# Kernel tuning notes

Measured on AMD Instinct MI355X. Metric: run time of the kernel, lower is better.

## Reference

```python
import jax, jax.numpy as jnp
import numpy as np
import math

DIM = 1024
K = 3
NUM_LAYERS = 1
RES_SCALE = 1.0 / math.sqrt(NUM_LAYERS)


def rmsnorm(x, gamma):
    # F.normalize(x, dim=-1) * sqrt(dim) * (gamma + 1)
    n = jnp.sqrt(jnp.sum(x * x, axis=-1, keepdims=True))
    return x / jnp.maximum(n, 1e-12) * (x.shape[-1] ** 0.5) * (gamma + 1.0)


def causal_dwconv(x, w_dw, b_dw, w_pw, b_pw):
    # x: [B, L, D]; w_dw: [D, 1, K]; w_pw: [D, D]
    xt = jnp.transpose(x, (0, 2, 1))                     # [B, D, L]
    xt = jnp.pad(xt, ((0, 0), (0, 0), (K - 1, 0)))       # causal left pad
    y = jax.lax.conv_general_dilated(
        xt, w_dw, window_strides=(1,), padding='VALID',
        feature_group_count=xt.shape[1],
        dimension_numbers=('NCH', 'OIH', 'NCH'))          # [B, D, L]
    y = y + b_dw[None, :, None]
    y = jnp.transpose(y, (0, 2, 1))                       # [B, L, D]
    return jnp.einsum('bld,ed->ble', y, w_pw) + b_pw      # 1x1 conv


def log_g(x):
    return jnp.where(x >= 0, jnp.log(jax.nn.relu(x) + 0.5), -jax.nn.softplus(-x))


def heinsen_scan_log(log_coeffs, log_values):
    # h_t = exp(a*_t + logcumsumexp(log_values - a*))
    a_star = jnp.cumsum(log_coeffs, axis=1)
    log_h = a_star + jax.lax.cumlogsumexp(log_values - a_star, axis=1)
    return jnp.exp(log_h)


def min_gru(x, w_hg):
    # x: [B, L, D]; w_hg: [2D, D] (no bias, expansion_factor=1 -> to_out is identity)
    hg = jnp.einsum('bld,ed->ble', x, w_hg)
    hidden, gate = jnp.split(hg, 2, axis=-1)
    log_coeffs = -jax.nn.softplus(gate)        # log(1 - z)
    log_values = -jax.nn.softplus(-gate) + log_g(hidden)  # log z + log g(h~)
    out = heinsen_scan_log(log_coeffs, log_values)         # [B, L, D]
    next_hidden = out[:, -1:]
    return out, next_hidden


def setup_inputs() -> dict:
    key = jax.random.key(0)
    ks = jax.random.split(key, 12)
    D = DIM
    s = 0.02
    return {
        'x': jax.random.normal(ks[0], (4, 4096, D), jnp.float32),
        'conv_dw_w': jax.random.normal(ks[1], (D, 1, K), jnp.float32) * s,
        'conv_dw_b': jax.random.normal(ks[2], (D,), jnp.float32) * s,
        'conv_pw_w': jax.random.normal(ks[3], (D, D), jnp.float32) * s,
        'conv_pw_b': jax.random.normal(ks[4], (D,), jnp.float32) * s,
        'conv_norm_g': jax.random.normal(ks[5], (D,), jnp.float32) * s,
        'gru_norm_g': jax.random.normal(ks[6], (D,), jnp.float32) * s,
        'gru_w': jax.random.normal(ks[7], (2 * D, D), jnp.float32) * s,
        'ff_norm_g': jax.random.normal(ks[8], (D,), jnp.float32) * s,
        'ff_w1': jax.random.normal(ks[9], (4 * D, D), jnp.float32) * s,
        'ff_b1': jax.random.normal(ks[10], (4 * D,), jnp.float32) * s,
        'ff_w2': jax.random.normal(ks[11], (D, 4 * D), jnp.float32) * s,
        'ff_b2': jnp.zeros((D,), jnp.float32),
    }


def reference(x, conv_dw_w, conv_dw_b, conv_pw_w, conv_pw_b, conv_norm_g,
              gru_norm_g, gru_w, ff_norm_g, ff_w1, ff_b1, ff_w2, ff_b2):
    # Conv branch (residual)
    x = causal_dwconv(rmsnorm(x, conv_norm_g), conv_dw_w, conv_dw_b,
                      conv_pw_w, conv_pw_b) * RES_SCALE + x
    # MinGRU branch (residual); dropout is identity at inference
    gru_out, next_hidden = min_gru(rmsnorm(x, gru_norm_g), gru_w)
    x = gru_out * RES_SCALE + x
    # FeedForward branch (residual), exact GELU
    h = rmsnorm(x, ff_norm_g)
    h = jax.nn.gelu(jnp.einsum('bld,ed->ble', h, ff_w1) + ff_b1, approximate=False)
    h = jnp.einsum('ble,de->bld', h, ff_w2) + ff_b2
    x = h * RES_SCALE + x
    return x, next_hidden
```

## Files before the change

kernel.cpp:

```cpp
#include <hip/hip_runtime.h>

typedef __attribute__((ext_vector_type(8))) short short8;
typedef __attribute__((ext_vector_type(4))) float floatx4;

#define D_   1024
#define L_   4096
#define B_   4
#define T_   16384
#define NCH  32
#define CHL  128

__device__ __forceinline__ ushort f2bf(float f) {
  unsigned u = __float_as_uint(f);
  u += 0x7fffu + ((u >> 16) & 1u);
  return (ushort)(u >> 16);
}
__device__ __forceinline__ float bf2f(ushort u) {
  return __uint_as_float(((unsigned)u) << 16);
}

__device__ __forceinline__ void gl2lds(const ushort* g, ushort* l) {
  __builtin_amdgcn_global_load_lds(
      (const __attribute__((address_space(1))) unsigned int*)g,
      (__attribute__((address_space(3))) unsigned int*)l, 16, 0, 0);
}

__global__ __launch_bounds__(256) void cvt_bf(const float* __restrict__ s,
                                              ushort* __restrict__ d, int n4) {
  int i = blockIdx.x * 256 + threadIdx.x;
  if (i >= n4) return;
  float4 v = ((const float4*)s)[i];
  ushort4 o;
  o.x = f2bf(v.x); o.y = f2bf(v.y); o.z = f2bf(v.z); o.w = f2bf(v.w);
  ((ushort4*)d)[i] = o;
}

__global__ __launch_bounds__(256) void rms_reduce(const float* __restrict__ x,
                                                  float* __restrict__ inv) {
  int t = blockIdx.x;
  float4 v = ((const float4*)(x + (size_t)t * D_))[threadIdx.x];
  float s = v.x * v.x + v.y * v.y + v.z * v.z + v.w * v.w;
#pragma unroll
  for (int off = 32; off > 0; off >>= 1) s += __shfl_xor(s, off, 64);
  __shared__ float red[4];
  if ((threadIdx.x & 63) == 0) red[threadIdx.x >> 6] = s;
  __syncthreads();
  if (threadIdx.x == 0)
    inv[t] = 32.0f / fmaxf(sqrtf(red[0] + red[1] + red[2] + red[3]), 1e-12f);
}

__global__ __launch_bounds__(256) void rms_scale(const float* __restrict__ x,
                                                 const float* __restrict__ g,
                                                 ushort* __restrict__ z) {
  int t = blockIdx.x;
  float4 v = ((const float4*)(x + (size_t)t * D_))[threadIdx.x];
  float s = v.x * v.x + v.y * v.y + v.z * v.z + v.w * v.w;
#pragma unroll
  for (int off = 32; off > 0; off >>= 1) s += __shfl_xor(s, off, 64);
  __shared__ float red[4];
  if ((threadIdx.x & 63) == 0) red[threadIdx.x >> 6] = s;
  __syncthreads();
  float iv = 32.0f / fmaxf(sqrtf(red[0] + red[1] + red[2] + red[3]), 1e-12f);
  float4 gg = ((const float4*)g)[threadIdx.x];
  ushort4 o;
  o.x = f2bf(v.x * iv * (gg.x + 1.f));
  o.y = f2bf(v.y * iv * (gg.y + 1.f));
  o.z = f2bf(v.z * iv * (gg.z + 1.f));
  o.w = f2bf(v.w * iv * (gg.w + 1.f));
  ((ushort4*)(z + (size_t)t * D_))[threadIdx.x] = o;
}

__global__ __launch_bounds__(256) void dwconv_k(const float* __restrict__ x,
                                                const float* __restrict__ inv,
                                                const float* __restrict__ wdw,
                                                const float* __restrict__ bdw,
                                                const float* __restrict__ gm,
                                                ushort* __restrict__ y) {
  int t = blockIdx.x;
  int c4 = threadIdx.x << 2;
  int l = t & (L_ - 1);
  const float* p0 = x + (size_t)t * D_ + c4;
  float i0 = inv[t], i1 = 0.f, i2 = 0.f;
  float4 v0 = *(const float4*)p0;
  float4 v1 = {0.f, 0.f, 0.f, 0.f}, v2 = {0.f, 0.f, 0.f, 0.f};
  if (l >= 1) { v1 = *(const float4*)(p0 - D_);     i1 = inv[t - 1]; }
  if (l >= 2) { v2 = *(const float4*)(p0 - 2 * D_); i2 = inv[t - 2]; }
  float a0[4] = {v0.x, v0.y, v0.z, v0.w};
  float a1[4] = {v1.x, v1.y, v1.z, v1.w};
  float a2[4] = {v2.x, v2.y, v2.z, v2.w};
  ushort r[4];
#pragma unroll
  for (int j = 0; j < 4; ++j) {
    int d = c4 + j;
    float w0 = wdw[d * 3 + 0], w1 = wdw[d * 3 + 1], w2 = wdw[d * 3 + 2];
    float s = w2 * a0[j] * i0 + w1 * a1[j] * i1 + w0 * a2[j] * i2;
    s = s * (gm[d] + 1.0f) + bdw[d];
    r[j] = f2bf(s);
  }
  ushort4 o; o.x = r[0]; o.y = r[1]; o.z = r[2]; o.w = r[3];
  *(ushort4*)(y + (size_t)t * D_ + c4) = o;
}

template <int MODE>
__global__ __launch_bounds__(256, 2) void gemm_k(
    const ushort* __restrict__ A, const ushort* __restrict__ W,
    const float* __restrict__ bias, const float* __restrict__ resid,
    float* __restrict__ outF, ushort* __restrict__ outB, int M, int N, int K) {
  __shared__ ushort lA[128 * 32];
  __shared__ ushort lB[128 * 32];
  int tid = threadIdx.x;

  int nx = gridDim.x;
  int lxs = 31 - __clz(nx);
  int lin = blockIdx.x + blockIdx.y * nx;
  int c = lin & 7, q = lin >> 3;
  int by = (c * (gridDim.y >> 3)) + (q >> lxs);
  int bx = q & (nx - 1);
  int bm = by * 128;
  int bn = bx * 128;

  int wave = tid >> 6, lane = tid & 63;
  int wm = (wave & 1) << 6, wn = (wave >> 1) << 6;
  int row = tid >> 2, kc = (tid & 3) << 3;
  const ushort* pa0 = A + (size_t)(bm + row) * K + kc;
  const ushort* pa1 = pa0 + (size_t)64 * K;
  const ushort* pb0 = W + (size_t)(bn + row) * K + kc;
  const ushort* pb1 = pb0 + (size_t)64 * K;
  ushort* dA0 = lA + tid * 8;
  ushort* dA1 = dA0 + 64 * 32;
  ushort* dB0 = lB + tid * 8;
  ushort* dB1 = dB0 + 64 * 32;
  int fr = lane & 15, fq = lane >> 4;

  floatx4 acc[4][4];
#pragma unroll
  for (int i = 0; i < 4; ++i)
#pragma unroll
    for (int j = 0; j < 4; ++j) acc[i][j] = {0.f, 0.f, 0.f, 0.f};

  for (int k0 = 0; k0 < K; k0 += 32) {
    __syncthreads();
    gl2lds(pa0 + k0, dA0);
    gl2lds(pa1 + k0, dA1);
    gl2lds(pb0 + k0, dB0);
    gl2lds(pb1 + k0, dB1);
    __syncthreads();
    short8 af[4], bfr[4];
#pragma unroll
    for (int i = 0; i < 4; ++i)
      af[i] = *(const short8*)(lA + (wm + i * 16 + fr) * 32 + fq * 8);
#pragma unroll
    for (int j = 0; j < 4; ++j)
      bfr[j] = *(const short8*)(lB + (wn + j * 16 + fr) * 32 + fq * 8);
#pragma unroll
    for (int i = 0; i < 4; ++i)
#pragma unroll
      for (int j = 0; j < 4; ++j)
        acc[i][j] = __builtin_amdgcn_mfma_f32_16x16x32_bf16(af[i], bfr[j], acc[i][j], 0, 0, 0);
  }

#pragma unroll
  for (int i = 0; i < 4; ++i) {
#pragma unroll
    for (int j = 0; j < 4; ++j) {
      int colg = bn + wn + j * 16 + fr;
      float bv = (MODE == 3) ? 0.f : bias[colg];
#pragma unroll
      for (int r = 0; r < 4; ++r) {
        int rowg = bm + wm + i * 16 + fq * 4 + r;
        size_t idx = (size_t)rowg * N + colg;
        float v = acc[i][j][r];
        if (MODE == 0) {
          outF[idx] = v + bv + resid[idx];
        } else if (MODE == 2) {
          v += bv;
          v = 0.5f * v * (1.0f + erff(v * 0.70710678118f));
          outB[idx] = f2bf(v);
        } else {
          outB[idx] = f2bf(v);
        }
      }
    }
  }
}

__device__ __forceinline__ void gates(float hid, float gt, float& a, float& bv) {
  a = 1.f / (1.f + __expf(gt));
  float sg = 1.f / (1.f + __expf(-gt));
  float g = (hid >= 0.f) ? (hid + 0.5f) : (1.f / (1.f + __expf(-hid)));
  bv = sg * g;
}

__global__ __launch_bounds__(256) void scan_p1(const ushort* __restrict__ hg,
                                               float* __restrict__ Ag,
                                               float* __restrict__ Bg) {
  int blk = blockIdx.x;
  int dt = blk & 3, ch = (blk >> 2) & 31, b = blk >> 7;
  int d = (dt << 8) + threadIdx.x;
  const ushort* p = hg + (size_t)(b * L_ + ch * CHL) * 2048 + d;
  float A = 1.f, Bv = 0.f;
  for (int s = 0; s < CHL; ++s) {
    float hid = bf2f(p[0]), gt = bf2f(p[1024]);
    p += 2048;
    float a, bv; gates(hid, gt, a, bv);
    A *= a;
    Bv = fmaf(a, Bv, bv);
  }
  size_t o = (size_t)((b * NCH + ch) * D_) + d;
  Ag[o] = A; Bg[o] = Bv;
}

__global__ __launch_bounds__(256) void scan_p2(const float* __restrict__ Ag,
                                               const float* __restrict__ Bg,
                                               float* __restrict__ Pre) {
  int dt = blockIdx.x & 3, b = blockIdx.x >> 2;
  int d = (dt << 8) + threadIdx.x;
  float h = 0.f;
  for (int c = 0; c < NCH; ++c) {
    size_t i = (size_t)((b * NCH + c) * D_) + d;
    Pre[i] = h;
    h = fmaf(Ag[i], h, Bg[i]);
  }
}

__global__ __launch_bounds__(256) void scan_p3(const ushort* __restrict__ hg,
                                               const float* __restrict__ Pre,
                                               float* __restrict__ xio,
                                               float* __restrict__ nh) {
  int blk = blockIdx.x;
  int dt = blk & 3, ch = (blk >> 2) & 31, b = blk >> 7;
  int d = (dt << 8) + threadIdx.x;
  const ushort* p = hg + (size_t)(b * L_ + ch * CHL) * 2048 + d;
  float* q = xio + (size_t)(b * L_ + ch * CHL) * D_ + d;
  float h = Pre[(size_t)((b * NCH + ch) * D_) + d];
  for (int s = 0; s < CHL; ++s) {
    float hid = bf2f(p[0]), gt = bf2f(p[1024]);
    p += 2048;
    float a, bv; gates(hid, gt, a, bv);
    h = fmaf(a, h, bv);
    *q = h + *q;
    q += D_;
  }
  if (ch == NCH - 1) nh[(b << 10) + d] = h;
}

extern "C" void kernel_launch(void* const* d_in, const int* in_sizes, int n_in,
                              void* d_out, int out_size, void* d_ws, size_t ws_size,
                              hipStream_t stream) {
  const float* x   = (const float*)d_in[0];
  const float* cdw = (const float*)d_in[1];
  const float* cdb = (const float*)d_in[2];
  const float* cpw = (const float*)d_in[3];
  const float* cpb = (const float*)d_in[4];
  const float* cng = (const float*)d_in[5];
  const float* gng = (const float*)d_in[6];
  const float* gw  = (const float*)d_in[7];
  const float* fng = (const float*)d_in[8];
  const float* fw1 = (const float*)d_in[9];
  const float* fb1 = (const float*)d_in[10];
  const float* fw2 = (const float*)d_in[11];
  const float* fb2 = (const float*)d_in[12];
  float* out = (float*)d_out;
  char* ws = (char*)d_ws;

  ushort* wpw_b = (ushort*)(ws + 0);
  ushort* wgr_b = (ushort*)(ws + 2097152);
  ushort* wf1_b = (ushort*)(ws + 6291456);
  ushort* wf2_b = (ushort*)(ws + 14680064);
  float*  inv   = (float*) (ws + 23068672);
  float*  Ag    = (float*) (ws + 23134208);
  float*  Bg    = (float*) (ws + 23658496);
  float*  Pre   = (float*) (ws + 24182784);
  ushort* zbuf  = (ushort*)(ws + 24707072);
  ushort* hg    = (ushort*)(ws + 58261504);
  ushort* h1    = (ushort*)(ws + 58261504);
  float*  nh    = out + (size_t)T_ * D_;

  cvt_bf<<<dim3(1024), 256, 0, stream>>>(cpw, wpw_b, 262144);
  cvt_bf<<<dim3(2048), 256, 0, stream>>>(gw,  wgr_b, 524288);
  cvt_bf<<<dim3(4096), 256, 0, stream>>>(fw1, wf1_b, 1048576);
  cvt_bf<<<dim3(4096), 256, 0, stream>>>(fw2, wf2_b, 1048576);

  rms_reduce<<<dim3(T_), 256, 0, stream>>>(x, inv);
  dwconv_k<<<dim3(T_), 256, 0, stream>>>(x, inv, cdw, cdb, cng, zbuf);
  gemm_k<0><<<dim3(8, 128), 256, 0, stream>>>(zbuf, wpw_b, cpb, x, out, nullptr, T_, 1024, 1024);

  rms_scale<<<dim3(T_), 256, 0, stream>>>(out, gng, zbuf);
  gemm_k<3><<<dim3(16, 128), 256, 0, stream>>>(zbuf, wgr_b, nullptr, nullptr, nullptr, hg, T_, 2048, 1024);
  scan_p1<<<dim3(512), 256, 0, stream>>>(hg, Ag, Bg);
  scan_p2<<<dim3(16), 256, 0, stream>>>(Ag, Bg, Pre);
  scan_p3<<<dim3(512), 256, 0, stream>>>(hg, Pre, out, nh);

  rms_scale<<<dim3(T_), 256, 0, stream>>>(out, fng, zbuf);
  gemm_k<2><<<dim3(32, 128), 256, 0, stream>>>(zbuf, wf1_b, fb1, nullptr, nullptr, h1, T_, 4096, 1024);
  gemm_k<0><<<dim3(8, 128), 256, 0, stream>>>(h1, wf2_b, fb2, out, out, nullptr, T_, 1024, 4096);
}
```

Baseline: 838.0 us.

## Fuse RMS reduction into dwconv, move minGRU gates into GEMM epilogue, approximate GELU

Drops the separate rms_reduce pass: dwconv now recomputes the norms of the current and two previous rows through block reductions. The minGRU gate nonlinearities move into the gate GEMM epilogue, which stores g(h) and the coefficient a in bf16, so both scan passes read them directly instead of evaluating exponentials twice. Exact erf-based GELU is replaced by the tanh-form approximation written as a sigmoid. This cuts memory passes and transcendental work, but adds a numerical deviation from the exact GELU and stores the gate coefficient at bf16 precision.

```diff
diff --git a/kernel.cpp b/kernel.cpp
--- a/kernel.cpp
+++ b/kernel.cpp
@@ -33,20 +33,6 @@
   ushort4 o;
   o.x = f2bf(v.x); o.y = f2bf(v.y); o.z = f2bf(v.z); o.w = f2bf(v.w);
   ((ushort4*)d)[i] = o;
-}
-
-__global__ __launch_bounds__(256) void rms_reduce(const float* __restrict__ x,
-                                                  float* __restrict__ inv) {
-  int t = blockIdx.x;
-  float4 v = ((const float4*)(x + (size_t)t * D_))[threadIdx.x];
-  float s = v.x * v.x + v.y * v.y + v.z * v.z + v.w * v.w;
-#pragma unroll
-  for (int off = 32; off > 0; off >>= 1) s += __shfl_xor(s, off, 64);
-  __shared__ float red[4];
-  if ((threadIdx.x & 63) == 0) red[threadIdx.x >> 6] = s;
-  __syncthreads();
-  if (threadIdx.x == 0)
-    inv[t] = 32.0f / fmaxf(sqrtf(red[0] + red[1] + red[2] + red[3]), 1e-12f);
 }
 
 __global__ __launch_bounds__(256) void rms_scale(const float* __restrict__ x,
@@ -71,7 +57,6 @@
 }
 
 __global__ __launch_bounds__(256) void dwconv_k(const float* __restrict__ x,
-                                                const float* __restrict__ inv,
                                                 const float* __restrict__ wdw,
                                                 const float* __restrict__ bdw,
                                                 const float* __restrict__ gm,
@@ -80,11 +65,28 @@
   int c4 = threadIdx.x << 2;
   int l = t & (L_ - 1);
   const float* p0 = x + (size_t)t * D_ + c4;
-  float i0 = inv[t], i1 = 0.f, i2 = 0.f;
   float4 v0 = *(const float4*)p0;
   float4 v1 = {0.f, 0.f, 0.f, 0.f}, v2 = {0.f, 0.f, 0.f, 0.f};
-  if (l >= 1) { v1 = *(const float4*)(p0 - D_);     i1 = inv[t - 1]; }
-  if (l >= 2) { v2 = *(const float4*)(p0 - 2 * D_); i2 = inv[t - 2]; }
+  if (l >= 1) v1 = *(const float4*)(p0 - D_);
+  if (l >= 2) v2 = *(const float4*)(p0 - 2 * D_);
+  float s0 = v0.x * v0.x + v0.y * v0.y + v0.z * v0.z + v0.w * v0.w;
+  float s1 = v1.x * v1.x + v1.y * v1.y + v1.z * v1.z + v1.w * v1.w;
+  float s2 = v2.x * v2.x + v2.y * v2.y + v2.z * v2.z + v2.w * v2.w;
+#pragma unroll
+  for (int off = 32; off > 0; off >>= 1) {
+    s0 += __shfl_xor(s0, off, 64);
+    s1 += __shfl_xor(s1, off, 64);
+    s2 += __shfl_xor(s2, off, 64);
+  }
+  __shared__ float r0[4], r1[4], r2[4];
+  if ((threadIdx.x & 63) == 0) {
+    int w = threadIdx.x >> 6;
+    r0[w] = s0; r1[w] = s1; r2[w] = s2;
+  }
+  __syncthreads();
+  float i0 = 32.0f / fmaxf(sqrtf(r0[0] + r0[1] + r0[2] + r0[3]), 1e-12f);
+  float i1 = 32.0f / fmaxf(sqrtf(r1[0] + r1[1] + r1[2] + r1[3]), 1e-12f);
+  float i2 = 32.0f / fmaxf(sqrtf(r2[0] + r2[1] + r2[2] + r2[3]), 1e-12f);
   float a0[4] = {v0.x, v0.y, v0.z, v0.w};
   float a1[4] = {v1.x, v1.y, v1.z, v1.w};
   float a2[4] = {v2.x, v2.y, v2.z, v2.w};
@@ -164,7 +166,7 @@
 #pragma unroll
     for (int j = 0; j < 4; ++j) {
       int colg = bn + wn + j * 16 + fr;
-      float bv = (MODE == 3) ? 0.f : bias[colg];
+      float bv = (MODE == 4) ? 0.f : bias[colg];
 #pragma unroll
       for (int r = 0; r < 4; ++r) {
         int rowg = bm + wm + i * 16 + fq * 4 + r;
@@ -174,21 +176,20 @@
           outF[idx] = v + bv + resid[idx];
         } else if (MODE == 2) {
           v += bv;
-          v = 0.5f * v * (1.0f + erff(v * 0.70710678118f));
+          float u = 1.5957691216f * (v + 0.044715f * v * v * v);
+          v = v / (1.f + __expf(-u));
           outB[idx] = f2bf(v);
         } else {
-          outB[idx] = f2bf(v);
+          float o;
+          if (colg < 1024)
+            o = (v >= 0.f) ? (v + 0.5f) : (1.f / (1.f + __expf(-v)));
+          else
+            o = 1.f / (1.f + __expf(v));
+          outB[idx] = f2bf(o);
         }
       }
     }
   }
-}
-
-__device__ __forceinline__ void gates(float hid, float gt, float& a, float& bv) {
-  a = 1.f / (1.f + __expf(gt));
-  float sg = 1.f / (1.f + __expf(-gt));
-  float g = (hid >= 0.f) ? (hid + 0.5f) : (1.f / (1.f + __expf(-hid)));
-  bv = sg * g;
 }
 
 __global__ __launch_bounds__(256) void scan_p1(const ushort* __restrict__ hg,
@@ -200,11 +201,10 @@
   const ushort* p = hg + (size_t)(b * L_ + ch * CHL) * 2048 + d;
   float A = 1.f, Bv = 0.f;
   for (int s = 0; s < CHL; ++s) {
-    float hid = bf2f(p[0]), gt = bf2f(p[1024]);
+    float g = bf2f(p[0]), a = bf2f(p[1024]);
     p += 2048;
-    float a, bv; gates(hid, gt, a, bv);
     A *= a;
-    Bv = fmaf(a, Bv, bv);
+    Bv = fmaf(a, Bv, (1.f - a) * g);
   }
   size_t o = (size_t)((b * NCH + ch) * D_) + d;
   Ag[o] = A; Bg[o] = Bv;
@@ -234,10 +234,9 @@
   float* q = xio + (size_t)(b * L_ + ch * CHL) * D_ + d;
   float h = Pre[(size_t)((b * NCH + ch) * D_) + d];
   for (int s = 0; s < CHL; ++s) {
-    float hid = bf2f(p[0]), gt = bf2f(p[1024]);
+    float g = bf2f(p[0]), a = bf2f(p[1024]);
     p += 2048;
-    float a, bv; gates(hid, gt, a, bv);
-    h = fmaf(a, h, bv);
+    h = fmaf(a, h, (1.f - a) * g);
     *q = h + *q;
     q += D_;
   }
@@ -267,7 +266,6 @@
   ushort* wgr_b = (ushort*)(ws + 2097152);
   ushort* wf1_b = (ushort*)(ws + 6291456);
   ushort* wf2_b = (ushort*)(ws + 14680064);
-  float*  inv   = (float*) (ws + 23068672);
   float*  Ag    = (float*) (ws + 23134208);
   float*  Bg    = (float*) (ws + 23658496);
   float*  Pre   = (float*) (ws + 24182784);
@@ -281,12 +279,11 @@
   cvt_bf<<<dim3(4096), 256, 0, stream>>>(fw1, wf1_b, 1048576);
   cvt_bf<<<dim3(4096), 256, 0, stream>>>(fw2, wf2_b, 1048576);
 
-  rms_reduce<<<dim3(T_), 256, 0, stream>>>(x, inv);
-  dwconv_k<<<dim3(T_), 256, 0, stream>>>(x, inv, cdw, cdb, cng, zbuf);
+  dwconv_k<<<dim3(T_), 256, 0, stream>>>(x, cdw, cdb, cng, zbuf);
   gemm_k<0><<<dim3(8, 128), 256, 0, stream>>>(zbuf, wpw_b, cpb, x, out, nullptr, T_, 1024, 1024);
 
   rms_scale<<<dim3(T_), 256, 0, stream>>>(out, gng, zbuf);
-  gemm_k<3><<<dim3(16, 128), 256, 0, stream>>>(zbuf, wgr_b, nullptr, nullptr, nullptr, hg, T_, 2048, 1024);
+  gemm_k<4><<<dim3(16, 128), 256, 0, stream>>>(zbuf, wgr_b, nullptr, nullptr, nullptr, hg, T_, 2048, 1024);
   scan_p1<<<dim3(512), 256, 0, stream>>>(hg, Ag, Bg);
   scan_p2<<<dim3(16), 256, 0, stream>>>(Ag, Bg, Pre);
   scan_p3<<<dim3(512), 256, 0, stream>>>(hg, Pre, out, nh);
```

New measurement: 733.1 us. 12.5% less time.
